# Performance work log

Hardware: AMD Instinct MI355X
Metric: run time of the kernel (lower is better)

The kernel has to match this reference:

```python
import jax, jax.numpy as jnp
import numpy as np

N_NODES = 50000
NODE_DIM = 128
HIDDEN = 256
BLOCK_OUT = 128
NUM_CLASSES = 40
N_EDGES = 800000


def setup_inputs() -> dict:
    key = jax.random.key(0)
    ks = jax.random.split(key, 12)
    glorot = lambda k, fi, fo: jax.random.normal(k, (fi, fo), jnp.float32) * (2.0 / (fi + fo)) ** 0.5
    return {
        "x": jax.random.normal(ks[0], (N_NODES, NODE_DIM), jnp.float32),
        "edge_index": jax.random.randint(ks[1], (2, N_EDGES), 0, N_NODES, jnp.int64),
        # block1: Node2Edge MLP (2*node_dim -> hidden), Edge2Node MLP (hidden -> 128)
        "W1": glorot(ks[2], 2 * NODE_DIM, HIDDEN),
        "b1": jnp.zeros((HIDDEN,), jnp.float32),
        "W2": glorot(ks[3], HIDDEN, BLOCK_OUT),
        "b2": jnp.zeros((BLOCK_OUT,), jnp.float32),
        # final Node2Edge: Linear(2*128,128) -> ReLU -> Linear(128,num_classes) -> LogSoftmax
        "W3": glorot(ks[4], 2 * BLOCK_OUT, 128),
        "b3": jnp.zeros((128,), jnp.float32),
        "W4": glorot(ks[5], 128, NUM_CLASSES),
        "b4": jnp.zeros((NUM_CLASSES,), jnp.float32),
    }


def reference(x, edge_index, W1, b1, W2, b2, W3, b3, W4, b4):
    src, dst = edge_index[0], edge_index[1]
    # Node2Edge: gather endpoints, concat, edge MLP
    e = jnp.concatenate([x[src], x[dst]], axis=-1)          # [E, 2*node_dim]
    eh = jax.nn.relu(e @ W1 + b1)                            # [E, hidden]
    # Edge2Node: scatter-mean edge features to destination nodes
    agg = jax.ops.segment_sum(eh, dst, num_segments=N_NODES)
    cnt = jax.ops.segment_sum(jnp.ones((eh.shape[0],), eh.dtype), dst, num_segments=N_NODES)
    mean = agg / jnp.maximum(cnt, 1.0)[:, None]              # [N, hidden]
    h = jax.nn.relu(mean @ W2 + b2)                          # [N, 128]
    # final Node2Edge head -> per-edge class log-probs
    e2 = jnp.concatenate([h[src], h[dst]], axis=-1)          # [E, 256]
    z = jax.nn.relu(e2 @ W3 + b3)                            # [E, 128]
    logits = z @ W4 + b4                                     # [E, num_classes]
    return jax.nn.log_softmax(logits, axis=-1)
```

## Files before the change

### kernel.cpp

```cpp
#include <hip/hip_runtime.h>
#include <hip/hip_bf16.h>


typedef short bf16x8 __attribute__((ext_vector_type(8)));
typedef float f32x4 __attribute__((ext_vector_type(4)));

#define N_NODES 50000
#define N_EDGES 800000

__device__ __forceinline__ unsigned short f2bf(float f) {
  unsigned u = __builtin_bit_cast(unsigned, f);
  u = u + 0x7fffu + ((u >> 16) & 1u);
  return (unsigned short)(u >> 16);
}
__device__ __forceinline__ float bf2f(unsigned short h) {
  unsigned u = ((unsigned)h) << 16;
  return __builtin_bit_cast(float, u);
}
__device__ __forceinline__ int ld_src(const int* ei, int m64, int e) {
  return m64 ? ei[2 * e] : ei[e];
}
__device__ __forceinline__ int ld_dst(const int* ei, int m64, int e) {
  return m64 ? ei[2 * N_EDGES + 2 * e] : ei[N_EDGES + e];
}

__global__ void k_prep_frags(const float* __restrict__ W1, const float* __restrict__ W2,
                             const float* __restrict__ W3, const float* __restrict__ W4,
                             const float* __restrict__ b4,
                             unsigned short* __restrict__ w1f, unsigned short* __restrict__ w2f,
                             unsigned short* __restrict__ w3f, unsigned short* __restrict__ w4f,
                             float* __restrict__ b4p, int* __restrict__ flagp,
                             const int* __restrict__ ei) {
  int gid = blockIdx.x * 256 + threadIdx.x;
  if (gid < 65536) {
    int i = gid & 7, lane = (gid >> 3) & 63, ks = (gid >> 9) & 3, ct = gid >> 11;
    int k = ks * 32 + (lane >> 4) * 8 + i;
    int c = ct * 16 + (lane & 15);
    float v = (c < 256) ? W1[k * 256 + c] : W1[(128 + k) * 256 + (c - 256)];
    w1f[gid] = f2bf(v);
  } else if (gid < 98304) {
    int f = gid - 65536;
    int i = f & 7, lane = (f >> 3) & 63, ks = (f >> 9) & 7, ct = f >> 12;
    int k = ks * 32 + (lane >> 4) * 8 + i;
    int c = ct * 16 + (lane & 15);
    w2f[f] = f2bf(W2[k * 128 + c]);
  } else if (gid < 131072) {
    int f = gid - 98304;
    int i = f & 7, lane = (f >> 3) & 63, ks = (f >> 9) & 3, ct = f >> 11;
    int k = ks * 32 + (lane >> 4) * 8 + i;
    int c = ct * 16 + (lane & 15);
    float v = (c < 128) ? W3[k * 128 + c] : W3[(128 + k) * 128 + (c - 128)];
    w3f[f] = f2bf(v);
  } else if (gid < 137216) {
    int f = gid - 131072;
    int i = f & 7, lane = (f >> 3) & 63, ks = (f >> 9) & 3, ct = f >> 11;
    int k = ks * 32 + (lane >> 4) * 8 + i;
    int c = ct * 16 + (lane & 15);
    w4f[f] = (c < 40) ? f2bf(W4[k * 40 + c]) : (unsigned short)0;
  } else if (gid < 137264) {
    int c = gid - 137216;
    b4p[c] = (c < 40) ? b4[c] : 0.f;
  } else if (gid == 137264) {
    *flagp = (ei[1] == 0 && ei[3] == 0 && ei[5] == 0 && ei[7] == 0) ? 1 : 0;
  }
}

__global__ void k_hist(const int* __restrict__ ei, const int* __restrict__ flagp,
                       int* __restrict__ hist) {
  int e = blockIdx.x * 256 + threadIdx.x;
  atomicAdd(&hist[ld_dst(ei, *flagp, e)], 1);
}

__global__ __launch_bounds__(256) void k_scan_a(const int* __restrict__ hist,
                                                int* __restrict__ bsum) {
  __shared__ int ps[256];
  int t = threadIdx.x, idx = blockIdx.x * 256 + t;
  ps[t] = (idx < N_NODES) ? hist[idx] : 0;
  __syncthreads();
  for (int off = 128; off > 0; off >>= 1) {
    if (t < off) ps[t] += ps[t + off];
    __syncthreads();
  }
  if (t == 0) bsum[blockIdx.x] = ps[0];
}

__global__ __launch_bounds__(256) void k_scan_b(int* __restrict__ bsum, int* __restrict__ seg) {
  __shared__ int ps[256];
  int t = threadIdx.x;
  int v = (t < 196) ? bsum[t] : 0;
  ps[t] = v;
  __syncthreads();
  for (int off = 1; off < 256; off <<= 1) {
    int u = (t >= off) ? ps[t - off] : 0;
    __syncthreads();
    ps[t] += u;
    __syncthreads();
  }
  if (t < 196) bsum[t] = ps[t] - v;
  if (t == 195) seg[N_NODES] = ps[195];
}

__global__ __launch_bounds__(256) void k_scan_c(int* __restrict__ hist,
                                                const int* __restrict__ bsum,
                                                int* __restrict__ seg) {
  __shared__ int ps[256];
  int t = threadIdx.x, idx = blockIdx.x * 256 + t;
  int v = (idx < N_NODES) ? hist[idx] : 0;
  ps[t] = v;
  __syncthreads();
  for (int off = 1; off < 256; off <<= 1) {
    int u = (t >= off) ? ps[t - off] : 0;
    __syncthreads();
    ps[t] += u;
    __syncthreads();
  }
  int run = bsum[blockIdx.x] + ps[t] - v;
  if (idx < N_NODES) {
    seg[idx] = run;
    hist[idx] = run;
  }
}

__global__ void k_scatter(const int* __restrict__ ei, const int* __restrict__ flagp,
                          int* __restrict__ cursor, int* __restrict__ ssrc) {
  int e = blockIdx.x * 256 + threadIdx.x;
  int m64 = *flagp;
  int s = ld_src(ei, m64, e), d = ld_dst(ei, m64, e);
  int pos = atomicAdd(&cursor[d], 1);
  ssrc[pos] = s;
}

__global__ __launch_bounds__(512, 2) void k_sy(const float* __restrict__ x,
                                               const unsigned short* __restrict__ w1f,
                                               const float* __restrict__ b1,
                                               unsigned short* __restrict__ SY) {
  __shared__ __attribute__((aligned(16))) short A[64 * 128];
  const int t = threadIdx.x;
  const int nb = blockIdx.x * 64;
  const int nv = min(64, N_NODES - nb);
  const int w = t >> 6, l = t & 63, lr = l & 15, lh = l >> 4;

  bf16x8 B[4][4];
#pragma unroll
  for (int ci = 0; ci < 4; ++ci)
#pragma unroll
    for (int ks = 0; ks < 4; ++ks)
      B[ci][ks] = *(const bf16x8*)(w1f + (((w * 4 + ci) * 4 + ks) * 64 + l) * 8);

#pragma unroll
  for (int j = 0; j < 2; ++j) {
    int c = t + 512 * j;
    int row = c >> 4, ck = c & 15;
    int rr = (row < nv) ? row : 0;
    const float* gp = x + (long)(nb + rr) * 128 + ck * 8;
    float4 v0 = *(const float4*)gp;
    float4 v1 = *(const float4*)(gp + 4);
    bf16x8 o;
    o[0] = (short)f2bf(v0.x); o[1] = (short)f2bf(v0.y);
    o[2] = (short)f2bf(v0.z); o[3] = (short)f2bf(v0.w);
    o[4] = (short)f2bf(v1.x); o[5] = (short)f2bf(v1.y);
    o[6] = (short)f2bf(v1.z); o[7] = (short)f2bf(v1.w);
    int off = (row << 8) + (ck << 4);
    off ^= (row & 7) << 4;
    *(bf16x8*)((char*)A + off) = o;
  }
  __syncthreads();

#pragma unroll
  for (int rt = 0; rt < 4; ++rt) {
    f32x4 acc[4] = {};
#pragma unroll
    for (int ks = 0; ks < 4; ++ks) {
      int row = rt * 16 + lr;
      int off = (row << 8) + (ks << 6) + (lh << 4);
      off ^= (row & 7) << 4;
      bf16x8 a = *(const bf16x8*)((const char*)A + off);
#pragma unroll
      for (int ci = 0; ci < 4; ++ci)
        acc[ci] = __builtin_amdgcn_mfma_f32_16x16x32_bf16(a, B[ci][ks], acc[ci], 0, 0, 0);
    }
#pragma unroll
    for (int ci = 0; ci < 4; ++ci) {
      int col = (w * 4 + ci) * 16 + lr;
      float bb = (col >= 256) ? b1[col - 256] : 0.f;
#pragma unroll
      for (int r = 0; r < 4; ++r) {
        int row = rt * 16 + lh * 4 + r;
        if (row < nv) SY[(long)(nb + row) * 512 + col] = f2bf(acc[ci][r] + bb);
      }
    }
  }
}

__global__ __launch_bounds__(512) void k_edge_agg(unsigned short* __restrict__ SY,
                                                  const int* __restrict__ seg,
                                                  const int* __restrict__ ssrc) {
  const int t = threadIdx.x, w = t >> 6, l = t & 63;
  const int d = blockIdx.x * 8 + w;
  const int s0 = seg[d], s1 = seg[d + 1];
  unsigned short* Yp = SY + (long)d * 512 + 256 + l * 4;
  ushort4 yu = *(const ushort4*)Yp;
  const float y0 = bf2f(yu.x), y1 = bf2f(yu.y), y2 = bf2f(yu.z), y3 = bf2f(yu.w);
  float a0 = 0.f, a1 = 0.f, a2 = 0.f, a3 = 0.f;
  int pos = s0;
  for (; pos + 4 <= s1; pos += 4) {
    int sA = ssrc[pos], sB = ssrc[pos + 1], sC = ssrc[pos + 2], sD = ssrc[pos + 3];
    ushort4 uA = *(const ushort4*)(SY + (long)sA * 512 + l * 4);
    ushort4 uB = *(const ushort4*)(SY + (long)sB * 512 + l * 4);
    ushort4 uC = *(const ushort4*)(SY + (long)sC * 512 + l * 4);
    ushort4 uD = *(const ushort4*)(SY + (long)sD * 512 + l * 4);
    a0 += fmaxf(bf2f(uA.x) + y0, 0.f); a1 += fmaxf(bf2f(uA.y) + y1, 0.f);
    a2 += fmaxf(bf2f(uA.z) + y2, 0.f); a3 += fmaxf(bf2f(uA.w) + y3, 0.f);
    a0 += fmaxf(bf2f(uB.x) + y0, 0.f); a1 += fmaxf(bf2f(uB.y) + y1, 0.f);
    a2 += fmaxf(bf2f(uB.z) + y2, 0.f); a3 += fmaxf(bf2f(uB.w) + y3, 0.f);
    a0 += fmaxf(bf2f(uC.x) + y0, 0.f); a1 += fmaxf(bf2f(uC.y) + y1, 0.f);
    a2 += fmaxf(bf2f(uC.z) + y2, 0.f); a3 += fmaxf(bf2f(uC.w) + y3, 0.f);
    a0 += fmaxf(bf2f(uD.x) + y0, 0.f); a1 += fmaxf(bf2f(uD.y) + y1, 0.f);
    a2 += fmaxf(bf2f(uD.z) + y2, 0.f); a3 += fmaxf(bf2f(uD.w) + y3, 0.f);
  }
  for (; pos < s1; ++pos) {
    int sA = ssrc[pos];
    ushort4 uA = *(const ushort4*)(SY + (long)sA * 512 + l * 4);
    a0 += fmaxf(bf2f(uA.x) + y0, 0.f); a1 += fmaxf(bf2f(uA.y) + y1, 0.f);
    a2 += fmaxf(bf2f(uA.z) + y2, 0.f); a3 += fmaxf(bf2f(uA.w) + y3, 0.f);
  }
  float inv = 1.0f / fmaxf((float)(s1 - s0), 1.0f);
  ushort4 o;
  o.x = f2bf(a0 * inv); o.y = f2bf(a1 * inv);
  o.z = f2bf(a2 * inv); o.w = f2bf(a3 * inv);
  *(ushort4*)Yp = o;
}

__global__ __launch_bounds__(256, 2) void k_pq(unsigned short* __restrict__ SY,
                                               const unsigned short* __restrict__ w2f,
                                               const float* __restrict__ b2,
                                               const unsigned short* __restrict__ w3f,
                                               const float* __restrict__ b3) {
  __shared__ __attribute__((aligned(16))) short M[64 * 256];
  __shared__ __attribute__((aligned(16))) short H[64 * 128];
  const int t = threadIdx.x;
  const int nb = blockIdx.x * 64;
  const int nv = min(64, N_NODES - nb);
  const int w = t >> 6, l = t & 63, lr = l & 15, lh = l >> 4;

  bf16x8 B2[2][8];
#pragma unroll
  for (int ci = 0; ci < 2; ++ci)
#pragma unroll
    for (int ks = 0; ks < 8; ++ks)
      B2[ci][ks] = *(const bf16x8*)(w2f + (((w * 2 + ci) * 8 + ks) * 64 + l) * 8);

#pragma unroll
  for (int j = 0; j < 8; ++j) {
    int c = t + 256 * j;
    int row = c >> 5, ck = c & 31;
    int rr = (row < nv) ? row : 0;
    int4 v = *(const int4*)(SY + (long)(nb + rr) * 512 + 256 + ck * 8);
    int off = (row << 9) + (ck << 4);
    off ^= (row & 7) << 4;
    *(int4*)((char*)M + off) = v;
  }
  __syncthreads();

#pragma unroll
  for (int rt = 0; rt < 4; ++rt) {
    f32x4 acc[2] = {};
#pragma unroll
    for (int ks = 0; ks < 8; ++ks) {
      int row = rt * 16 + lr;
      int off = (row << 9) + (ks << 6) + (lh << 4);
      off ^= (row & 7) << 4;
      bf16x8 a = *(const bf16x8*)((const char*)M + off);
      acc[0] = __builtin_amdgcn_mfma_f32_16x16x32_bf16(a, B2[0][ks], acc[0], 0, 0, 0);
      acc[1] = __builtin_amdgcn_mfma_f32_16x16x32_bf16(a, B2[1][ks], acc[1], 0, 0, 0);
    }
#pragma unroll
    for (int ci = 0; ci < 2; ++ci) {
      int col = (w * 2 + ci) * 16 + lr;
      float bb = b2[col];
#pragma unroll
      for (int r = 0; r < 4; ++r) {
        int row = rt * 16 + lh * 4 + r;
        int off = (row << 8) + (col << 1);
        off ^= (row & 7) << 4;
        *(short*)((char*)H + off) = (short)f2bf(fmaxf(acc[ci][r] + bb, 0.f));
      }
    }
  }
  __syncthreads();

  bf16x8 B3[4][4];
#pragma unroll
  for (int ci = 0; ci < 4; ++ci)
#pragma unroll
    for (int ks = 0; ks < 4; ++ks)
      B3[ci][ks] = *(const bf16x8*)(w3f + (((w * 4 + ci) * 4 + ks) * 64 + l) * 8);

#pragma unroll
  for (int rt = 0; rt < 4; ++rt) {
    f32x4 acc[4] = {};
#pragma unroll
    for (int ks = 0; ks < 4; ++ks) {
      int row = rt * 16 + lr;
      int off = (row << 8) + (ks << 6) + (lh << 4);
      off ^= (row & 7) << 4;
      bf16x8 a = *(const bf16x8*)((const char*)H + off);
#pragma unroll
      for (int ci = 0; ci < 4; ++ci)
        acc[ci] = __builtin_amdgcn_mfma_f32_16x16x32_bf16(a, B3[ci][ks], acc[ci], 0, 0, 0);
    }
#pragma unroll
    for (int ci = 0; ci < 4; ++ci) {
      int col = (w * 4 + ci) * 16 + lr;
      float bb = (col >= 128) ? b3[col - 128] : 0.f;
#pragma unroll
      for (int r = 0; r < 4; ++r) {
        int row = rt * 16 + lh * 4 + r;
        if (row < nv) SY[(long)(nb + row) * 512 + col] = f2bf(acc[ci][r] + bb);
      }
    }
  }
}

__global__ __launch_bounds__(256, 2) void k_head(const unsigned short* __restrict__ SY,
                                                 const int* __restrict__ ei,
                                                 const unsigned short* __restrict__ w4f,
                                                 const float* __restrict__ b4p,
                                                 float* __restrict__ out,
                                                 const int* __restrict__ flagp) {
  const int t = threadIdx.x, w = t >> 6, l = t & 63, lr = l & 15, lh = l >> 4;
  const int m64 = *flagp;
  const int eb = blockIdx.x * 64 + w * 16;
  const int el = eb + lr;
  const int sn = ld_src(ei, m64, el);
  const int dn = ld_dst(ei, m64, el);
  const unsigned short* Pp = SY + (long)sn * 512;
  const unsigned short* Qp = SY + (long)dn * 512 + 128;

  bf16x8 B4[3][4];
#pragma unroll
  for (int ci = 0; ci < 3; ++ci)
#pragma unroll
    for (int ks = 0; ks < 4; ++ks)
      B4[ci][ks] = *(const bf16x8*)(w4f + ((ci * 4 + ks) * 64 + l) * 8);

  f32x4 acc[3] = {};
#pragma unroll
  for (int ks = 0; ks < 4; ++ks) {
    bf16x8 p = *(const bf16x8*)(Pp + ks * 32 + lh * 8);
    bf16x8 q = *(const bf16x8*)(Qp + ks * 32 + lh * 8);
    bf16x8 a;
#pragma unroll
    for (int i = 0; i < 8; ++i)
      a[i] = (short)f2bf(fmaxf(bf2f((unsigned short)p[i]) + bf2f((unsigned short)q[i]), 0.f));
#pragma unroll
    for (int ci = 0; ci < 3; ++ci)
      acc[ci] = __builtin_amdgcn_mfma_f32_16x16x32_bf16(a, B4[ci][ks], acc[ci], 0, 0, 0);
  }

  float lg0[4], lg1[4], lg2[4];
  const bool val2 = lr < 8;
  const float bb0 = b4p[lr], bb1 = b4p[16 + lr], bb2 = b4p[32 + lr];
#pragma unroll
  for (int r = 0; r < 4; ++r) {
    lg0[r] = acc[0][r] + bb0;
    lg1[r] = acc[1][r] + bb1;
    lg2[r] = acc[2][r] + bb2;
  }
#pragma unroll
  for (int r = 0; r < 4; ++r) {
    float m = fmaxf(lg0[r], lg1[r]);
    if (val2) m = fmaxf(m, lg2[r]);
    m = fmaxf(m, __shfl_xor(m, 1, 64));
    m = fmaxf(m, __shfl_xor(m, 2, 64));
    m = fmaxf(m, __shfl_xor(m, 4, 64));
    m = fmaxf(m, __shfl_xor(m, 8, 64));
    float s = __expf(lg0[r] - m) + __expf(lg1[r] - m) + (val2 ? __expf(lg2[r] - m) : 0.f);
    s += __shfl_xor(s, 1, 64);
    s += __shfl_xor(s, 2, 64);
    s += __shfl_xor(s, 4, 64);
    s += __shfl_xor(s, 8, 64);
    float lse = m + __logf(s);
    long ob = (long)(eb + lh * 4 + r) * 40;
    out[ob + lr] = lg0[r] - lse;
    out[ob + 16 + lr] = lg1[r] - lse;
    if (val2) out[ob + 32 + lr] = lg2[r] - lse;
  }
}

extern "C" void kernel_launch(void* const* d_in, const int* in_sizes, int n_in,
                              void* d_out, int out_size, void* d_ws, size_t ws_size,
                              hipStream_t stream) {
  const float* x = (const float*)d_in[0];
  const int* ei = (const int*)d_in[1];
  const float* W1 = (const float*)d_in[2];
  const float* b1 = (const float*)d_in[3];
  const float* W2 = (const float*)d_in[4];
  const float* b2 = (const float*)d_in[5];
  const float* W3 = (const float*)d_in[6];
  const float* b3 = (const float*)d_in[7];
  const float* W4 = (const float*)d_in[8];
  const float* b4 = (const float*)d_in[9];
  char* ws = (char*)d_ws;
  int* hist = (int*)(ws + 0);
  int* seg = (int*)(ws + 200064);
  int* bsum = (int*)(ws + 400128);
  int* ssrc = (int*)(ws + 401152);
  unsigned short* SY = (unsigned short*)(ws + 3601408);
  unsigned short* w1f = (unsigned short*)(ws + 54801408);
  unsigned short* w2f = (unsigned short*)(ws + 54932480);
  unsigned short* w3f = (unsigned short*)(ws + 54998016);
  unsigned short* w4f = (unsigned short*)(ws + 55063552);
  float* b4p = (float*)(ws + 55075840);
  int* flagp = (int*)(ws + 55076032);
  float* out = (float*)d_out;

  hipMemsetAsync(ws, 0, 200000, stream);
  k_prep_frags<<<537, 256, 0, stream>>>(W1, W2, W3, W4, b4, w1f, w2f, w3f, w4f, b4p, flagp, ei);
  k_hist<<<3125, 256, 0, stream>>>(ei, flagp, hist);
  k_scan_a<<<196, 256, 0, stream>>>(hist, bsum);
  k_scan_b<<<1, 256, 0, stream>>>(bsum, seg);
  k_scan_c<<<196, 256, 0, stream>>>(hist, bsum, seg);
  k_scatter<<<3125, 256, 0, stream>>>(ei, flagp, hist, ssrc);
  k_sy<<<782, 512, 0, stream>>>(x, w1f, b1, SY);
  k_edge_agg<<<6250, 512, 0, stream>>>(SY, seg, ssrc);
  k_pq<<<782, 256, 0, stream>>>(SY, w2f, b2, w3f, b3);
  k_head<<<12500, 256, 0, stream>>>(SY, ei, w4f, b4p, out, flagp);
}
```

Measured before the change: 307.8 us.

## Fuse scan and scatter kernels, split SY buffer, deepen gather unroll

Several changes land together. The single-block scan_b is folded into scan_c, with each block redoing the small 196-entry prefix scan itself, and the edge scatter shares one launch with the node GEMM k_sy as separate block ranges. The interleaved 512-wide SY buffer becomes two 256-wide buffers (S and Ypr), so edge_agg gathers from a denser array. The edge_agg gather loop is unrolled to 8 outstanding loads, and the flag kernel is replaced by an inline 64-bit probe. k_head gains perm-based bf16 packing (truncation instead of round-to-nearest) and nontemporal output stores.

```diff
diff --git a/kernel.cpp b/kernel.cpp
--- a/kernel.cpp
+++ b/kernel.cpp
@@ -16,6 +16,13 @@
 __device__ __forceinline__ float bf2f(unsigned short h) {
   unsigned u = ((unsigned)h) << 16;
   return __builtin_bit_cast(float, u);
+}
+__device__ __forceinline__ unsigned pack2(float lo, float hi) {
+  return __builtin_amdgcn_perm(__builtin_bit_cast(unsigned, hi),
+                               __builtin_bit_cast(unsigned, lo), 0x07060302u);
+}
+__device__ __forceinline__ int probe64(const int* ei) {
+  return (ei[1] == 0 && ei[3] == 0 && ei[5] == 0 && ei[7] == 0) ? 1 : 0;
 }
 __device__ __forceinline__ int ld_src(const int* ei, int m64, int e) {
   return m64 ? ei[2 * e] : ei[e];
@@ -29,8 +36,7 @@
                              const float* __restrict__ b4,
                              unsigned short* __restrict__ w1f, unsigned short* __restrict__ w2f,
                              unsigned short* __restrict__ w3f, unsigned short* __restrict__ w4f,
-                             float* __restrict__ b4p, int* __restrict__ flagp,
-                             const int* __restrict__ ei) {
+                             float* __restrict__ b4p) {
   int gid = blockIdx.x * 256 + threadIdx.x;
   if (gid < 65536) {
     int i = gid & 7, lane = (gid >> 3) & 63, ks = (gid >> 9) & 3, ct = gid >> 11;
@@ -60,15 +66,12 @@
   } else if (gid < 137264) {
     int c = gid - 137216;
     b4p[c] = (c < 40) ? b4[c] : 0.f;
-  } else if (gid == 137264) {
-    *flagp = (ei[1] == 0 && ei[3] == 0 && ei[5] == 0 && ei[7] == 0) ? 1 : 0;
-  }
-}
-
-__global__ void k_hist(const int* __restrict__ ei, const int* __restrict__ flagp,
-                       int* __restrict__ hist) {
+  }
+}
+
+__global__ void k_hist(const int* __restrict__ ei, int* __restrict__ hist) {
   int e = blockIdx.x * 256 + threadIdx.x;
-  atomicAdd(&hist[ld_dst(ei, *flagp, e)], 1);
+  atomicAdd(&hist[ld_dst(ei, probe64(ei), e)], 1);
 }
 
 __global__ __launch_bounds__(256) void k_scan_a(const int* __restrict__ hist,
@@ -84,10 +87,23 @@
   if (t == 0) bsum[blockIdx.x] = ps[0];
 }
 
-__global__ __launch_bounds__(256) void k_scan_b(int* __restrict__ bsum, int* __restrict__ seg) {
+__global__ __launch_bounds__(256) void k_scan_c(int* __restrict__ hist,
+                                                const int* __restrict__ bsum,
+                                                int* __restrict__ seg) {
+  __shared__ int bs[256];
   __shared__ int ps[256];
-  int t = threadIdx.x;
-  int v = (t < 196) ? bsum[t] : 0;
+  int t = threadIdx.x, idx = blockIdx.x * 256 + t;
+  bs[t] = (t < 196) ? bsum[t] : 0;
+  __syncthreads();
+  for (int off = 1; off < 256; off <<= 1) {
+    int u = (t >= off) ? bs[t - off] : 0;
+    __syncthreads();
+    bs[t] += u;
+    __syncthreads();
+  }
+  const int base = (blockIdx.x == 0) ? 0 : bs[blockIdx.x - 1];
+  if (blockIdx.x == 0 && t == 0) seg[N_NODES] = bs[195];
+  int v = (idx < N_NODES) ? hist[idx] : 0;
   ps[t] = v;
   __syncthreads();
   for (int off = 1; off < 256; off <<= 1) {
@@ -96,47 +112,31 @@
     ps[t] += u;
     __syncthreads();
   }
-  if (t < 196) bsum[t] = ps[t] - v;
-  if (t == 195) seg[N_NODES] = ps[195];
-}
-
-__global__ __launch_bounds__(256) void k_scan_c(int* __restrict__ hist,
-                                                const int* __restrict__ bsum,
-                                                int* __restrict__ seg) {
-  __shared__ int ps[256];
-  int t = threadIdx.x, idx = blockIdx.x * 256 + t;
-  int v = (idx < N_NODES) ? hist[idx] : 0;
-  ps[t] = v;
-  __syncthreads();
-  for (int off = 1; off < 256; off <<= 1) {
-    int u = (t >= off) ? ps[t - off] : 0;
-    __syncthreads();
-    ps[t] += u;
-    __syncthreads();
-  }
-  int run = bsum[blockIdx.x] + ps[t] - v;
+  int run = base + ps[t] - v;
   if (idx < N_NODES) {
     seg[idx] = run;
     hist[idx] = run;
   }
 }
 
-__global__ void k_scatter(const int* __restrict__ ei, const int* __restrict__ flagp,
-                          int* __restrict__ cursor, int* __restrict__ ssrc) {
-  int e = blockIdx.x * 256 + threadIdx.x;
-  int m64 = *flagp;
-  int s = ld_src(ei, m64, e), d = ld_dst(ei, m64, e);
-  int pos = atomicAdd(&cursor[d], 1);
-  ssrc[pos] = s;
-}
-
-__global__ __launch_bounds__(512, 2) void k_sy(const float* __restrict__ x,
-                                               const unsigned short* __restrict__ w1f,
-                                               const float* __restrict__ b1,
-                                               unsigned short* __restrict__ SY) {
+__global__ __launch_bounds__(512, 2) void k_scatter_sy(
+    const int* __restrict__ ei, int* __restrict__ cursor, int* __restrict__ ssrc,
+    const float* __restrict__ x, const unsigned short* __restrict__ w1f,
+    const float* __restrict__ b1, unsigned short* __restrict__ S,
+    unsigned short* __restrict__ Ypr) {
+  const int t = threadIdx.x;
+  if (blockIdx.x < 1563) {
+    int e = blockIdx.x * 512 + t;
+    if (e < N_EDGES) {
+      int m64 = probe64(ei);
+      int s = ld_src(ei, m64, e), d = ld_dst(ei, m64, e);
+      int pos = atomicAdd(&cursor[d], 1);
+      ssrc[pos] = s;
+    }
+    return;
+  }
   __shared__ __attribute__((aligned(16))) short A[64 * 128];
-  const int t = threadIdx.x;
-  const int nb = blockIdx.x * 64;
+  const int nb = (blockIdx.x - 1563) * 64;
   const int nv = min(64, N_NODES - nb);
   const int w = t >> 6, l = t & 63, lr = l & 15, lh = l >> 4;
 
@@ -182,47 +182,55 @@
 #pragma unroll
     for (int ci = 0; ci < 4; ++ci) {
       int col = (w * 4 + ci) * 16 + lr;
-      float bb = (col >= 256) ? b1[col - 256] : 0.f;
 #pragma unroll
       for (int r = 0; r < 4; ++r) {
         int row = rt * 16 + lh * 4 + r;
-        if (row < nv) SY[(long)(nb + row) * 512 + col] = f2bf(acc[ci][r] + bb);
+        if (row < nv) {
+          if (col < 256) {
+            S[(long)(nb + row) * 256 + col] = f2bf(acc[ci][r]);
+          } else {
+            Ypr[(long)(nb + row) * 256 + (col - 256)] = f2bf(acc[ci][r] + b1[col - 256]);
+          }
+        }
       }
     }
   }
 }
 
-__global__ __launch_bounds__(512) void k_edge_agg(unsigned short* __restrict__ SY,
+__global__ __launch_bounds__(512) void k_edge_agg(const unsigned short* __restrict__ S,
+                                                  unsigned short* __restrict__ Ypr,
                                                   const int* __restrict__ seg,
                                                   const int* __restrict__ ssrc) {
   const int t = threadIdx.x, w = t >> 6, l = t & 63;
   const int d = blockIdx.x * 8 + w;
   const int s0 = seg[d], s1 = seg[d + 1];
-  unsigned short* Yp = SY + (long)d * 512 + 256 + l * 4;
+  unsigned short* Yp = Ypr + (long)d * 256 + l * 4;
   ushort4 yu = *(const ushort4*)Yp;
   const float y0 = bf2f(yu.x), y1 = bf2f(yu.y), y2 = bf2f(yu.z), y3 = bf2f(yu.w);
   float a0 = 0.f, a1 = 0.f, a2 = 0.f, a3 = 0.f;
   int pos = s0;
-  for (; pos + 4 <= s1; pos += 4) {
-    int sA = ssrc[pos], sB = ssrc[pos + 1], sC = ssrc[pos + 2], sD = ssrc[pos + 3];
-    ushort4 uA = *(const ushort4*)(SY + (long)sA * 512 + l * 4);
-    ushort4 uB = *(const ushort4*)(SY + (long)sB * 512 + l * 4);
-    ushort4 uC = *(const ushort4*)(SY + (long)sC * 512 + l * 4);
-    ushort4 uD = *(const ushort4*)(SY + (long)sD * 512 + l * 4);
-    a0 += fmaxf(bf2f(uA.x) + y0, 0.f); a1 += fmaxf(bf2f(uA.y) + y1, 0.f);
-    a2 += fmaxf(bf2f(uA.z) + y2, 0.f); a3 += fmaxf(bf2f(uA.w) + y3, 0.f);
-    a0 += fmaxf(bf2f(uB.x) + y0, 0.f); a1 += fmaxf(bf2f(uB.y) + y1, 0.f);
-    a2 += fmaxf(bf2f(uB.z) + y2, 0.f); a3 += fmaxf(bf2f(uB.w) + y3, 0.f);
-    a0 += fmaxf(bf2f(uC.x) + y0, 0.f); a1 += fmaxf(bf2f(uC.y) + y1, 0.f);
-    a2 += fmaxf(bf2f(uC.z) + y2, 0.f); a3 += fmaxf(bf2f(uC.w) + y3, 0.f);
-    a0 += fmaxf(bf2f(uD.x) + y0, 0.f); a1 += fmaxf(bf2f(uD.y) + y1, 0.f);
-    a2 += fmaxf(bf2f(uD.z) + y2, 0.f); a3 += fmaxf(bf2f(uD.w) + y3, 0.f);
+  for (; pos + 8 <= s1; pos += 8) {
+    ushort4 u[8];
+#pragma unroll
+    for (int j = 0; j < 8; ++j) {
+      int s = ssrc[pos + j];
+      u[j] = *(const ushort4*)(S + (long)s * 256 + l * 4);
+    }
+#pragma unroll
+    for (int j = 0; j < 8; ++j) {
+      a0 += fmaxf(bf2f(u[j].x) + y0, 0.f);
+      a1 += fmaxf(bf2f(u[j].y) + y1, 0.f);
+      a2 += fmaxf(bf2f(u[j].z) + y2, 0.f);
+      a3 += fmaxf(bf2f(u[j].w) + y3, 0.f);
+    }
   }
   for (; pos < s1; ++pos) {
-    int sA = ssrc[pos];
-    ushort4 uA = *(const ushort4*)(SY + (long)sA * 512 + l * 4);
-    a0 += fmaxf(bf2f(uA.x) + y0, 0.f); a1 += fmaxf(bf2f(uA.y) + y1, 0.f);
-    a2 += fmaxf(bf2f(uA.z) + y2, 0.f); a3 += fmaxf(bf2f(uA.w) + y3, 0.f);
+    int s = ssrc[pos];
+    ushort4 uA = *(const ushort4*)(S + (long)s * 256 + l * 4);
+    a0 += fmaxf(bf2f(uA.x) + y0, 0.f);
+    a1 += fmaxf(bf2f(uA.y) + y1, 0.f);
+    a2 += fmaxf(bf2f(uA.z) + y2, 0.f);
+    a3 += fmaxf(bf2f(uA.w) + y3, 0.f);
   }
   float inv = 1.0f / fmaxf((float)(s1 - s0), 1.0f);
   ushort4 o;
@@ -231,7 +239,8 @@
   *(ushort4*)Yp = o;
 }
 
-__global__ __launch_bounds__(256, 2) void k_pq(unsigned short* __restrict__ SY,
+__global__ __launch_bounds__(256, 2) void k_pq(const unsigned short* __restrict__ Ypr,
+                                               unsigned short* __restrict__ PQ,
                                                const unsigned short* __restrict__ w2f,
                                                const float* __restrict__ b2,
                                                const unsigned short* __restrict__ w3f,
@@ -255,7 +264,7 @@
     int c = t + 256 * j;
     int row = c >> 5, ck = c & 31;
     int rr = (row < nv) ? row : 0;
-    int4 v = *(const int4*)(SY + (long)(nb + rr) * 512 + 256 + ck * 8);
+    int4 v = *(const int4*)(Ypr + (long)(nb + rr) * 256 + ck * 8);
     int off = (row << 9) + (ck << 4);
     off ^= (row & 7) << 4;
     *(int4*)((char*)M + off) = v;
@@ -316,26 +325,25 @@
 #pragma unroll
       for (int r = 0; r < 4; ++r) {
         int row = rt * 16 + lh * 4 + r;
-        if (row < nv) SY[(long)(nb + row) * 512 + col] = f2bf(acc[ci][r] + bb);
+        if (row < nv) PQ[(long)(nb + row) * 256 + col] = f2bf(acc[ci][r] + bb);
       }
     }
   }
 }
 
-__global__ __launch_bounds__(256, 2) void k_head(const unsigned short* __restrict__ SY,
+__global__ __launch_bounds__(256, 2) void k_head(const unsigned short* __restrict__ PQ,
                                                  const int* __restrict__ ei,
                                                  const unsigned short* __restrict__ w4f,
                                                  const float* __restrict__ b4p,
-                                                 float* __restrict__ out,
-                                                 const int* __restrict__ flagp) {
+                                                 float* __restrict__ out) {
   const int t = threadIdx.x, w = t >> 6, l = t & 63, lr = l & 15, lh = l >> 4;
-  const int m64 = *flagp;
+  const int m64 = probe64(ei);
   const int eb = blockIdx.x * 64 + w * 16;
   const int el = eb + lr;
   const int sn = ld_src(ei, m64, el);
   const int dn = ld_dst(ei, m64, el);
-  const unsigned short* Pp = SY + (long)sn * 512;
-  const unsigned short* Qp = SY + (long)dn * 512 + 128;
+  const unsigned short* Pp = PQ + (long)sn * 256;
+  const unsigned short* Qp = PQ + (long)dn * 256 + 128;
 
   bf16x8 B4[3][4];
 #pragma unroll
@@ -349,10 +357,14 @@
   for (int ks = 0; ks < 4; ++ks) {
     bf16x8 p = *(const bf16x8*)(Pp + ks * 32 + lh * 8);
     bf16x8 q = *(const bf16x8*)(Qp + ks * 32 + lh * 8);
-    bf16x8 a;
+    float f[8];
 #pragma unroll
     for (int i = 0; i < 8; ++i)
-      a[i] = (short)f2bf(fmaxf(bf2f((unsigned short)p[i]) + bf2f((unsigned short)q[i]), 0.f));
+      f[i] = fmaxf(bf2f((unsigned short)p[i]) + bf2f((unsigned short)q[i]), 0.f);
+    int4 a4;
+    a4.x = pack2(f[0], f[1]); a4.y = pack2(f[2], f[3]);
+    a4.z = pack2(f[4], f[5]); a4.w = pack2(f[6], f[7]);
+    bf16x8 a = __builtin_bit_cast(bf16x8, a4);
 #pragma unroll
     for (int ci = 0; ci < 3; ++ci)
       acc[ci] = __builtin_amdgcn_mfma_f32_16x16x32_bf16(a, B4[ci][ks], acc[ci], 0, 0, 0);
@@ -382,9 +394,9 @@
     s += __shfl_xor(s, 8, 64);
     float lse = m + __logf(s);
     long ob = (long)(eb + lh * 4 + r) * 40;
-    out[ob + lr] = lg0[r] - lse;
-    out[ob + 16 + lr] = lg1[r] - lse;
-    if (val2) out[ob + 32 + lr] = lg2[r] - lse;
+    __builtin_nontemporal_store(lg0[r] - lse, &out[ob + lr]);
+    __builtin_nontemporal_store(lg1[r] - lse, &out[ob + 16 + lr]);
+    if (val2) __builtin_nontemporal_store(lg2[r] - lse, &out[ob + 32 + lr]);
   }
 }
 
@@ -406,24 +418,22 @@
   int* seg = (int*)(ws + 200064);
   int* bsum = (int*)(ws + 400128);
   int* ssrc = (int*)(ws + 401152);
-  unsigned short* SY = (unsigned short*)(ws + 3601408);
+  unsigned short* S = (unsigned short*)(ws + 3601408);
+  unsigned short* Ypr = (unsigned short*)(ws + 29201408);
   unsigned short* w1f = (unsigned short*)(ws + 54801408);
   unsigned short* w2f = (unsigned short*)(ws + 54932480);
   unsigned short* w3f = (unsigned short*)(ws + 54998016);
   unsigned short* w4f = (unsigned short*)(ws + 55063552);
   float* b4p = (float*)(ws + 55075840);
-  int* flagp = (int*)(ws + 55076032);
   float* out = (float*)d_out;
 
   hipMemsetAsync(ws, 0, 200000, stream);
-  k_prep_frags<<<537, 256, 0, stream>>>(W1, W2, W3, W4, b4, w1f, w2f, w3f, w4f, b4p, flagp, ei);
-  k_hist<<<3125, 256, 0, stream>>>(ei, flagp, hist);
+  k_prep_frags<<<537, 256, 0, stream>>>(W1, W2, W3, W4, b4, w1f, w2f, w3f, w4f, b4p);
+  k_hist<<<3125, 256, 0, stream>>>(ei, hist);
   k_scan_a<<<196, 256, 0, stream>>>(hist, bsum);
-  k_scan_b<<<1, 256, 0, stream>>>(bsum, seg);
   k_scan_c<<<196, 256, 0, stream>>>(hist, bsum, seg);
-  k_scatter<<<3125, 256, 0, stream>>>(ei, flagp, hist, ssrc);
-  k_sy<<<782, 512, 0, stream>>>(x, w1f, b1, SY);
-  k_edge_agg<<<6250, 512, 0, stream>>>(SY, seg, ssrc);
-  k_pq<<<782, 256, 0, stream>>>(SY, w2f, b2, w3f, b3);
-  k_head<<<12500, 256, 0, stream>>>(SY, ei, w4f, b4p, out, flagp);
-}
+  k_scatter_sy<<<2345, 512, 0, stream>>>(ei, hist, ssrc, x, w1f, b1, S, Ypr);
+  k_edge_agg<<<6250, 512, 0, stream>>>(S, Ypr, seg, ssrc);
+  k_pq<<<782, 256, 0, stream>>>(Ypr, S, w2f, b2, w3f, b3);
+  k_head<<<12500, 256, 0, stream>>>(S, ei, w4f, b4p, out);
+}
```

After: 319.6 us. +3.8%, slower.
